# Kernel optimization log

Measured on AMD Instinct MI355X. Metric: run time of the kernel, lower is better.

Reference implementation:

```python
import jax, jax.numpy as jnp
import numpy as np

N_NODES = 8192
IN_F = 256
OUT_F = 256
ALPHA = 0.2  # LeakyReLU negative slope


def setup_inputs() -> dict:
    key = jax.random.key(0)
    k1, k2, k3, k4 = jax.random.split(key, 4)
    X = jax.random.normal(k1, (N_NODES, IN_F), dtype=jnp.float32)
    A = jax.random.randint(k2, (N_NODES, N_NODES), 0, 2, dtype=jnp.int32)
    # torch nn.Linear weight layout: (out_features, in_features)
    W = jax.random.normal(k3, (OUT_F, IN_F), dtype=jnp.float32) * (1.0 / np.sqrt(IN_F))
    r = jax.random.normal(k4, (2 * OUT_F, 1), dtype=jnp.float32)
    return {"X": X, "A": A, "W": W, "r": r}


def reference(X, A, W, r):
    # Wh = X @ W^T  -> (N, F_out)
    Wh = X @ W.T
    # Split r so that cat([Wh_i, Wh_j]) @ r == Wh_i @ r_src + Wh_j @ r_dst
    F_out = Wh.shape[-1]
    r_src = r[:F_out, 0]   # (F,)
    r_dst = r[F_out:, 0]   # (F,)
    s_i = Wh @ r_src       # (N,)
    s_j = Wh @ r_dst       # (N,)
    e = s_i[:, None] + s_j[None, :]                      # (N, N)
    e = jnp.where(e >= 0, e, ALPHA * e)                  # LeakyReLU
    e = jnp.where(A == 0, -jnp.inf, e)                   # mask non-edges
    attention = jax.nn.softmax(e, axis=1)                # row-wise softmax
    output = attention @ Wh                              # (N, F_out)
    return jax.nn.gelu(output, approximate=False)        # torch F.gelu (exact)
```

## Files before the change

kernel.cpp:

```cpp
#include <hip/hip_runtime.h>
#include <hip/hip_bf16.h>

#define N_NODES 8192
#define NF      256
#define L2E     1.44269504088896341f

typedef __attribute__((ext_vector_type(8))) short short8;
typedef __attribute__((ext_vector_type(4))) short short4v;
typedef __attribute__((ext_vector_type(4))) float floatx4;

static __device__ __forceinline__ float bf2f(short s) {
    return __uint_as_float(((unsigned)(unsigned short)s) << 16);
}
static __device__ __forceinline__ short f2bf_rn(float f) {
    unsigned u = __float_as_uint(f) + 0x8000u;
    return (short)(u >> 16);
}
struct bfpair { short hi, lo; };
static __device__ __forceinline__ bfpair split_bf(float x) {
    bfpair p;
    p.hi = f2bf_rn(x);
    p.lo = f2bf_rn(x - bf2f(p.hi));
    return p;
}
static __device__ __forceinline__ void async16(const void* g, void* l) {
    __builtin_amdgcn_global_load_lds(
        (const __attribute__((address_space(1))) unsigned*)g,
        (__attribute__((address_space(3))) unsigned*)l, 16, 0, 0);
}

__global__ __launch_bounds__(256) void kx_split(const float* __restrict__ W,
                                                short* __restrict__ Whi,
                                                short* __restrict__ Wlo) {
    #pragma unroll
    for (int e = 0; e < 4; ++e) {
        const int i = blockIdx.x * 1024 + e * 256 + threadIdx.x;
        bfpair p = split_bf(W[i]);
        Whi[i] = p.hi;
        Wlo[i] = p.lo;
    }
}

__global__ __launch_bounds__(512) void k1_gemm(const float* __restrict__ X,
                                               const short* __restrict__ Whi,
                                               const short* __restrict__ Wlo,
                                               const float* __restrict__ r,
                                               short* __restrict__ WhT,
                                               float* __restrict__ sp_src,
                                               float* __restrict__ sp_dst) {
    __shared__ float Xs[32 * 256];

    const int tid = threadIdx.x;
    const int w = tid >> 6, lane = tid & 63;
    const int q = lane >> 4, m = lane & 15;
    const int rh = w >> 2, cq = w & 3;
    const int i_base = blockIdx.x * 32;

    #pragma unroll
    for (int v = 0; v < 4; ++v) {
        const int rowv = w * 4 + v;
        const int c = lane ^ (rowv & 7);
        async16(X + (size_t)(i_base + rowv) * NF + c * 4, &Xs[rowv * 256]);
    }
    __syncthreads();

    floatx4 acc[4] = {};
    const int xrow = rh * 16 + m;
    const int r7 = xrow & 7;
    #pragma unroll
    for (int ks = 0; ks < 8; ++ks) {
        const int c0 = ks * 8 + q * 2;
        float4 f0 = *(const float4*)(&Xs[xrow * 256 + ((c0 ^ r7) * 4)]);
        float4 f1 = *(const float4*)(&Xs[xrow * 256 + (((c0 + 1) ^ r7) * 4)]);
        const float xsv[8] = {f0.x, f0.y, f0.z, f0.w, f1.x, f1.y, f1.z, f1.w};
        short8 xh, xl;
        #pragma unroll
        for (int c = 0; c < 8; ++c) {
            bfpair p = split_bf(xsv[c]);
            xh[c] = p.hi; xl[c] = p.lo;
        }
        #pragma unroll
        for (int nt = 0; nt < 4; ++nt) {
            const int n = cq * 64 + nt * 16 + m;
            short8 wh = *(const short8*)(Whi + n * NF + ks * 32 + q * 8);
            short8 wl = *(const short8*)(Wlo + n * NF + ks * 32 + q * 8);
            acc[nt] = __builtin_amdgcn_mfma_f32_16x16x32_bf16(xh, wh, acc[nt], 0, 0, 0);
            acc[nt] = __builtin_amdgcn_mfma_f32_16x16x32_bf16(xl, wh, acc[nt], 0, 0, 0);
            acc[nt] = __builtin_amdgcn_mfma_f32_16x16x32_bf16(xh, wl, acc[nt], 0, 0, 0);
        }
    }

    const int i0 = i_base + rh * 16 + q * 4;
    float vs[4] = {0.f, 0.f, 0.f, 0.f}, vd[4] = {0.f, 0.f, 0.f, 0.f};
    #pragma unroll
    for (int nt = 0; nt < 4; ++nt) {
        const int n = cq * 64 + nt * 16 + m;
        short4v v;
        #pragma unroll
        for (int r2 = 0; r2 < 4; ++r2) v[r2] = f2bf_rn(acc[nt][r2]);
        *(short4v*)(WhT + (size_t)n * N_NODES + i0) = v;
        const float rs = r[n], rd = r[NF + n];
        #pragma unroll
        for (int r2 = 0; r2 < 4; ++r2) {
            vs[r2] = fmaf(acc[nt][r2], rs, vs[r2]);
            vd[r2] = fmaf(acc[nt][r2], rd, vd[r2]);
        }
    }
    #pragma unroll
    for (int mask = 1; mask <= 8; mask <<= 1) {
        #pragma unroll
        for (int r2 = 0; r2 < 4; ++r2) {
            vs[r2] += __shfl_xor(vs[r2], mask);
            vd[r2] += __shfl_xor(vd[r2], mask);
        }
    }
    if (m == 0) {
        #pragma unroll
        for (int r2 = 0; r2 < 4; ++r2) {
            sp_src[cq * N_NODES + i0 + r2] = vs[r2];
            sp_dst[cq * N_NODES + i0 + r2] = vd[r2];
        }
    }
}

__global__ __launch_bounds__(256) void k2_sv(const float* __restrict__ sp_src,
                                             const float* __restrict__ sp_dst,
                                             float* __restrict__ s_src,
                                             float* __restrict__ s_dst,
                                             float* __restrict__ pmax) {
    __shared__ float red[256];
    const int tid = threadIdx.x;
    const int i = blockIdx.x * 256 + tid;
    float ss = 0.f, sd = 0.f;
    #pragma unroll
    for (int nb = 0; nb < 4; ++nb) {
        ss += sp_src[nb * N_NODES + i];
        sd += sp_dst[nb * N_NODES + i];
    }
    s_src[i] = ss;
    s_dst[i] = sd;
    red[tid] = sd;
    __syncthreads();
    for (int off = 128; off > 0; off >>= 1) {
        if (tid < off) red[tid] = fmaxf(red[tid], red[tid + off]);
        __syncthreads();
    }
    if (tid == 0) pmax[blockIdx.x] = red[0];
}

__global__ __launch_bounds__(512) void k3_bits(const int* __restrict__ Adj,
                                               unsigned* __restrict__ mask) {
    const int w = threadIdx.x >> 6, lane = threadIdx.x & 63;
    const int row = blockIdx.x * 8 + w;
    const int* Ar = Adj + (size_t)row * N_NODES;
    unsigned long long* Mr = (unsigned long long*)(mask + (size_t)row * 256);
    for (int it = 0; it < 128; ++it) {
        const int v = Ar[it * 64 + lane];
        const unsigned long long b = __ballot(v != 0);
        if (lane == 0) Mr[it] = b;
    }
}

static __device__ __forceinline__ void pgroupb(const unsigned bits, const int sh,
                                               const floatx4 t,
                                               const float s_i, const float d_i,
                                               float* p) {
    #pragma unroll
    for (int c = 0; c < 4; ++c) {
        float sum = s_i + t[c];
        float lr  = fmaxf(sum, 0.2f * sum);
        float pp  = __builtin_amdgcn_exp2f(fmaf(lr, L2E, d_i));
        p[c] = ((bits >> (sh + c)) & 1u) ? pp : 0.0f;
    }
}

__global__ __launch_bounds__(512, 4) void k4_attn(const unsigned* __restrict__ Abits,
                                                  const short* __restrict__ WhT,
                                                  const float* __restrict__ s_dst,
                                                  const float* __restrict__ s_src,
                                                  const float* __restrict__ pmax,
                                                  float* __restrict__ pden,
                                                  float* __restrict__ outacc) {
    __shared__ short Bs[2][256][64];
    __shared__ float ts[2048];

    const int tid = threadIdx.x;
    const int w = tid >> 6, lane = tid & 63;
    const int q = lane >> 4, m = lane & 15;
    const int rh = w >> 1, ch = w & 1;
    const int ib = blockIdx.x & 127;
    const int jh = blockIdx.x >> 7;
    const int i0 = ib * 64;
    const int jbase = jh * 2048;
    const int row = i0 + rh * 16 + m;
    const int q8 = q * 8;

    float M = pmax[0];
    #pragma unroll
    for (int b = 1; b < 32; ++b) M = fmaxf(M, pmax[b]);
    const float s_i = s_src[row];
    const float e0 = s_i + M;
    const float d_i = -fmaxf(e0, 0.2f * e0) * L2E;

    const int srow = lane >> 3;
    const int scc = (lane & 7) ^ srow;
    const short* gB[4];
    #pragma unroll
    for (int v = 0; v < 4; ++v)
        gB[v] = WhT + (size_t)(w * 32 + v * 8 + srow) * N_NODES + jbase + scc * 8;

    const unsigned* Mp = Abits + (size_t)row * 256 + (jbase >> 5);

    floatx4 acc[8];
    #pragma unroll
    for (int nt = 0; nt < 8; ++nt) acc[nt] = (floatx4){0.f, 0.f, 0.f, 0.f};
    float den = 0.f;

    async16(s_dst + jbase + w * 256 + lane * 4, &ts[w * 256]);
    #pragma unroll
    for (int v = 0; v < 4; ++v)
        async16(gB[v], &Bs[0][w * 32 + v * 8][0]);
    uint2 mk = *(const uint2*)(Mp);
    __syncthreads();

    for (int s = 0; s < 32; ++s) {
        const int cur = s & 1;

        short* dstb = &Bs[cur ^ 1][0][0];
        const int gn = ((s + 1) & 31) * 64;
        #pragma unroll
        for (int v = 0; v < 4; ++v)
            async16(gB[v] + gn, dstb + (w * 32 + v * 8) * 64);
        __builtin_amdgcn_sched_barrier(0);

        uint2 nmk = *(const uint2*)(Mp + ((s + 1) & 31) * 2);
        __builtin_amdgcn_sched_barrier(0);

        const int gt = s * 64;
        floatx4 t0 = *(const floatx4*)(ts + gt + q8);
        floatx4 t1 = *(const floatx4*)(ts + gt + q8 + 4);
        floatx4 t2 = *(const floatx4*)(ts + gt + 32 + q8);
        floatx4 t3 = *(const floatx4*)(ts + gt + 32 + q8 + 4);

        float p[16];
        pgroupb(mk.x, q8,     t0, s_i, d_i, p);
        pgroupb(mk.x, q8 + 4, t1, s_i, d_i, p + 4);
        pgroupb(mk.y, q8,     t2, s_i, d_i, p + 8);
        pgroupb(mk.y, q8 + 4, t3, s_i, d_i, p + 12);

        short8 af0, af1;
        #pragma unroll
        for (int c = 0; c < 8; ++c) { af0[c] = f2bf_rn(p[c]); af1[c] = f2bf_rn(p[8 + c]); }
        #pragma unroll
        for (int c = 0; c < 16; ++c) den += p[c];

        const short* Bb = &Bs[cur][0][0];
        __builtin_amdgcn_s_setprio(1);
        #pragma unroll
        for (int nt = 0; nt < 8; ++nt) {
            const int n = ch * 128 + nt * 16 + m;
            const int sw = m & 7;
            short8 b0 = *(const short8*)(Bb + n * 64 + ((q ^ sw) * 8));
            short8 b1 = *(const short8*)(Bb + n * 64 + (((4 + q) ^ sw) * 8));
            acc[nt] = __builtin_amdgcn_mfma_f32_16x16x32_bf16(af0, b0, acc[nt], 0, 0, 0);
            acc[nt] = __builtin_amdgcn_mfma_f32_16x16x32_bf16(af1, b1, acc[nt], 0, 0, 0);
        }
        __builtin_amdgcn_s_setprio(0);

        __builtin_amdgcn_sched_barrier(0);
        asm volatile("s_waitcnt vmcnt(1)" ::: "memory");
        __builtin_amdgcn_s_barrier();

        mk = nmk;
    }

    den += __shfl_xor(den, 16);
    den += __shfl_xor(den, 32);
    if (ch == 0 && q == 0) pden[jh * N_NODES + row] = den;

    #pragma unroll
    for (int nt = 0; nt < 8; ++nt) {
        #pragma unroll
        for (int rg = 0; rg < 4; ++rg) {
            const int orow = i0 + rh * 16 + q * 4 + rg;
            const int n = ch * 128 + nt * 16 + m;
            atomicAdd(&outacc[(size_t)orow * NF + n], acc[nt][rg]);
        }
    }
}

__global__ __launch_bounds__(256) void k5_fin(const float* __restrict__ pden,
                                              float* __restrict__ out) {
    const int gid = blockIdx.x * 256 + threadIdx.x;
    const int row = gid >> 5;
    const int c0 = (gid & 31) * 8;
    const float d = (pden[row] + pden[N_NODES + row]) +
                    (pden[2 * N_NODES + row] + pden[3 * N_NODES + row]);
    const float inv = 1.0f / fmaxf(d, 1e-30f);
    float* p = out + (size_t)row * NF + c0;
    float4 v0 = *(const float4*)(p);
    float4 v1 = *(const float4*)(p + 4);
    float xs[8] = {v0.x, v0.y, v0.z, v0.w, v1.x, v1.y, v1.z, v1.w};
    #pragma unroll
    for (int c = 0; c < 8; ++c) {
        const float x = xs[c] * inv;
        xs[c] = 0.5f * x * (1.0f + erff(x * 0.70710678118f));
    }
    *(float4*)(p)     = (float4){xs[0], xs[1], xs[2], xs[3]};
    *(float4*)(p + 4) = (float4){xs[4], xs[5], xs[6], xs[7]};
}

extern "C" void kernel_launch(void* const* d_in, const int* in_sizes, int n_in,
                              void* d_out, int out_size, void* d_ws, size_t ws_size,
                              hipStream_t stream) {
    const float* X = (const float*)d_in[0];
    const int*   A = (const int*)d_in[1];
    const float* W = (const float*)d_in[2];
    const float* r = (const float*)d_in[3];
    float* out = (float*)d_out;

    char* wsp = (char*)d_ws;
    short* WhT    = (short*)wsp;                    wsp += (size_t)NF * N_NODES * 2;
    short* Whi    = (short*)wsp;                    wsp += NF * NF * 2;
    short* Wlo    = (short*)wsp;                    wsp += NF * NF * 2;
    float* sp_src = (float*)wsp;                    wsp += 4 * N_NODES * 4;
    float* sp_dst = (float*)wsp;                    wsp += 4 * N_NODES * 4;
    float* s_src  = (float*)wsp;                    wsp += N_NODES * 4;
    float* s_dst  = (float*)wsp;                    wsp += N_NODES * 4;
    float* pmax   = (float*)wsp;                    wsp += 256;
    unsigned* Abits = (unsigned*)wsp;
    float* pden   = sp_src;

    hipMemsetAsync(out, 0, (size_t)N_NODES * NF * 4, stream);
    kx_split<<<64, 256, 0, stream>>>(W, Whi, Wlo);
    k1_gemm<<<256, 512, 0, stream>>>(X, Whi, Wlo, r, WhT, sp_src, sp_dst);
    k2_sv<<<32, 256, 0, stream>>>(sp_src, sp_dst, s_src, s_dst, pmax);
    k3_bits<<<1024, 512, 0, stream>>>(A, Abits);
    k4_attn<<<512, 512, 0, stream>>>(Abits, WhT, s_dst, s_src, pmax, pden, out);
    k5_fin<<<1024, 256, 0, stream>>>(pden, out);
}
```

Before: 521.6 us.

## Retile attention kernel to 128-row blocks with 8-way j split; vectorize adjacency bitpacking

The attention kernel now gives each block 128 rows, one 16-row stripe per wave, covering all 256 output columns, and splits the j range into 8 chunks of 1024 instead of 4 of 2048. Each B tile loaded into shared memory is therefore reused across twice as many rows, and each wave holds 16 accumulator tiles. The cost is more accumulator registers, twice as many atomic adds into the output, and 8 partial denominators for the final kernel to sum. Separately, the adjacency bitmask kernel now has each thread pack 32 entries with int4 loads instead of a per-wave ballot loop, to get wider memory accesses. The pden scratch area now holds 8×N floats and relies on sp_src and sp_dst being contiguous, which is fragile.

```diff
diff --git a/kernel.cpp b/kernel.cpp
--- a/kernel.cpp
+++ b/kernel.cpp
@@ -148,17 +148,20 @@
     if (tid == 0) pmax[blockIdx.x] = red[0];
 }
 
-__global__ __launch_bounds__(512) void k3_bits(const int* __restrict__ Adj,
+__global__ __launch_bounds__(256) void k3_bits(const int* __restrict__ Adj,
                                                unsigned* __restrict__ mask) {
-    const int w = threadIdx.x >> 6, lane = threadIdx.x & 63;
-    const int row = blockIdx.x * 8 + w;
-    const int* Ar = Adj + (size_t)row * N_NODES;
-    unsigned long long* Mr = (unsigned long long*)(mask + (size_t)row * 256);
-    for (int it = 0; it < 128; ++it) {
-        const int v = Ar[it * 64 + lane];
-        const unsigned long long b = __ballot(v != 0);
-        if (lane == 0) Mr[it] = b;
-    }
+    const int gid = blockIdx.x * 256 + threadIdx.x;
+    const int4* src = (const int4*)Adj + (size_t)gid * 8;
+    unsigned b = 0;
+    #pragma unroll
+    for (int c = 0; c < 8; ++c) {
+        const int4 v = src[c];
+        b |= (v.x != 0 ? 1u : 0u) << (c * 4);
+        b |= (v.y != 0 ? 1u : 0u) << (c * 4 + 1);
+        b |= (v.z != 0 ? 1u : 0u) << (c * 4 + 2);
+        b |= (v.w != 0 ? 1u : 0u) << (c * 4 + 3);
+    }
+    mask[gid] = b;
 }
 
 static __device__ __forceinline__ void pgroupb(const unsigned bits, const int sh,
@@ -182,16 +185,16 @@
                                                   float* __restrict__ pden,
                                                   float* __restrict__ outacc) {
     __shared__ short Bs[2][256][64];
-    __shared__ float ts[2048];
+    __shared__ float ts[1024];
 
     const int tid = threadIdx.x;
     const int w = tid >> 6, lane = tid & 63;
     const int q = lane >> 4, m = lane & 15;
-    const int rh = w >> 1, ch = w & 1;
-    const int ib = blockIdx.x & 127;
-    const int jh = blockIdx.x >> 7;
-    const int i0 = ib * 64;
-    const int jbase = jh * 2048;
+    const int rh = w;
+    const int ib = blockIdx.x & 63;
+    const int jh = blockIdx.x >> 6;
+    const int i0 = ib * 128;
+    const int jbase = jh * 1024;
     const int row = i0 + rh * 16 + m;
     const int q8 = q * 8;
 
@@ -211,61 +214,71 @@
 
     const unsigned* Mp = Abits + (size_t)row * 256 + (jbase >> 5);
 
-    floatx4 acc[8];
-    #pragma unroll
-    for (int nt = 0; nt < 8; ++nt) acc[nt] = (floatx4){0.f, 0.f, 0.f, 0.f};
+    floatx4 acc[16];
+    #pragma unroll
+    for (int nt = 0; nt < 16; ++nt) acc[nt] = (floatx4){0.f, 0.f, 0.f, 0.f};
     float den = 0.f;
 
-    async16(s_dst + jbase + w * 256 + lane * 4, &ts[w * 256]);
+    if (w < 4) async16(s_dst + jbase + w * 256 + lane * 4, &ts[w * 256]);
     #pragma unroll
     for (int v = 0; v < 4; ++v)
         async16(gB[v], &Bs[0][w * 32 + v * 8][0]);
     uint2 mk = *(const uint2*)(Mp);
     __syncthreads();
 
-    for (int s = 0; s < 32; ++s) {
+    for (int s = 0; s < 16; ++s) {
         const int cur = s & 1;
 
         short* dstb = &Bs[cur ^ 1][0][0];
-        const int gn = ((s + 1) & 31) * 64;
+        const int gn = ((s + 1) & 15) * 64;
         #pragma unroll
         for (int v = 0; v < 4; ++v)
             async16(gB[v] + gn, dstb + (w * 32 + v * 8) * 64);
         __builtin_amdgcn_sched_barrier(0);
 
-        uint2 nmk = *(const uint2*)(Mp + ((s + 1) & 31) * 2);
+        uint2 nmk = *(const uint2*)(Mp + ((s + 1) & 15) * 2);
         __builtin_amdgcn_sched_barrier(0);
 
         const int gt = s * 64;
-        floatx4 t0 = *(const floatx4*)(ts + gt + q8);
-        floatx4 t1 = *(const floatx4*)(ts + gt + q8 + 4);
-        floatx4 t2 = *(const floatx4*)(ts + gt + 32 + q8);
-        floatx4 t3 = *(const floatx4*)(ts + gt + 32 + q8 + 4);
-
-        float p[16];
-        pgroupb(mk.x, q8,     t0, s_i, d_i, p);
-        pgroupb(mk.x, q8 + 4, t1, s_i, d_i, p + 4);
-        pgroupb(mk.y, q8,     t2, s_i, d_i, p + 8);
-        pgroupb(mk.y, q8 + 4, t3, s_i, d_i, p + 12);
-
-        short8 af0, af1;
-        #pragma unroll
-        for (int c = 0; c < 8; ++c) { af0[c] = f2bf_rn(p[c]); af1[c] = f2bf_rn(p[8 + c]); }
-        #pragma unroll
-        for (int c = 0; c < 16; ++c) den += p[c];
-
         const short* Bb = &Bs[cur][0][0];
-        __builtin_amdgcn_s_setprio(1);
-        #pragma unroll
-        for (int nt = 0; nt < 8; ++nt) {
-            const int n = ch * 128 + nt * 16 + m;
-            const int sw = m & 7;
-            short8 b0 = *(const short8*)(Bb + n * 64 + ((q ^ sw) * 8));
-            short8 b1 = *(const short8*)(Bb + n * 64 + (((4 + q) ^ sw) * 8));
-            acc[nt] = __builtin_amdgcn_mfma_f32_16x16x32_bf16(af0, b0, acc[nt], 0, 0, 0);
-            acc[nt] = __builtin_amdgcn_mfma_f32_16x16x32_bf16(af1, b1, acc[nt], 0, 0, 0);
-        }
-        __builtin_amdgcn_s_setprio(0);
+        const int sw = m & 7;
+
+        {
+            floatx4 t0 = *(const floatx4*)(ts + gt + q8);
+            floatx4 t1 = *(const floatx4*)(ts + gt + q8 + 4);
+            float p[8];
+            pgroupb(mk.x, q8,     t0, s_i, d_i, p);
+            pgroupb(mk.x, q8 + 4, t1, s_i, d_i, p + 4);
+            short8 af0;
+            #pragma unroll
+            for (int c = 0; c < 8; ++c) { af0[c] = f2bf_rn(p[c]); den += p[c]; }
+            __builtin_amdgcn_s_setprio(1);
+            #pragma unroll
+            for (int nt = 0; nt < 16; ++nt) {
+                const int n = nt * 16 + m;
+                short8 b0 = *(const short8*)(Bb + n * 64 + ((q ^ sw) * 8));
+                acc[nt] = __builtin_amdgcn_mfma_f32_16x16x32_bf16(af0, b0, acc[nt], 0, 0, 0);
+            }
+            __builtin_amdgcn_s_setprio(0);
+        }
+        {
+            floatx4 t2 = *(const floatx4*)(ts + gt + 32 + q8);
+            floatx4 t3 = *(const floatx4*)(ts + gt + 32 + q8 + 4);
+            float p[8];
+            pgroupb(mk.y, q8,     t2, s_i, d_i, p);
+            pgroupb(mk.y, q8 + 4, t3, s_i, d_i, p + 4);
+            short8 af1;
+            #pragma unroll
+            for (int c = 0; c < 8; ++c) { af1[c] = f2bf_rn(p[c]); den += p[c]; }
+            __builtin_amdgcn_s_setprio(1);
+            #pragma unroll
+            for (int nt = 0; nt < 16; ++nt) {
+                const int n = nt * 16 + m;
+                short8 b1 = *(const short8*)(Bb + n * 64 + (((4 + q) ^ sw) * 8));
+                acc[nt] = __builtin_amdgcn_mfma_f32_16x16x32_bf16(af1, b1, acc[nt], 0, 0, 0);
+            }
+            __builtin_amdgcn_s_setprio(0);
+        }
 
         __builtin_amdgcn_sched_barrier(0);
         asm volatile("s_waitcnt vmcnt(1)" ::: "memory");
@@ -276,14 +289,14 @@
 
     den += __shfl_xor(den, 16);
     den += __shfl_xor(den, 32);
-    if (ch == 0 && q == 0) pden[jh * N_NODES + row] = den;
-
-    #pragma unroll
-    for (int nt = 0; nt < 8; ++nt) {
+    if (q == 0) pden[jh * N_NODES + row] = den;
+
+    #pragma unroll
+    for (int nt = 0; nt < 16; ++nt) {
         #pragma unroll
         for (int rg = 0; rg < 4; ++rg) {
             const int orow = i0 + rh * 16 + q * 4 + rg;
-            const int n = ch * 128 + nt * 16 + m;
+            const int n = nt * 16 + m;
             atomicAdd(&outacc[(size_t)orow * NF + n], acc[nt][rg]);
         }
     }
@@ -294,8 +307,10 @@
     const int gid = blockIdx.x * 256 + threadIdx.x;
     const int row = gid >> 5;
     const int c0 = (gid & 31) * 8;
-    const float d = (pden[row] + pden[N_NODES + row]) +
-                    (pden[2 * N_NODES + row] + pden[3 * N_NODES + row]);
+    const float d = ((pden[row] + pden[N_NODES + row]) +
+                     (pden[2 * N_NODES + row] + pden[3 * N_NODES + row])) +
+                    ((pden[4 * N_NODES + row] + pden[5 * N_NODES + row]) +
+                     (pden[6 * N_NODES + row] + pden[7 * N_NODES + row]));
     const float inv = 1.0f / fmaxf(d, 1e-30f);
     float* p = out + (size_t)row * NF + c0;
     float4 v0 = *(const float4*)(p);
@@ -335,7 +350,7 @@
     kx_split<<<64, 256, 0, stream>>>(W, Whi, Wlo);
     k1_gemm<<<256, 512, 0, stream>>>(X, Whi, Wlo, r, WhT, sp_src, sp_dst);
     k2_sv<<<32, 256, 0, stream>>>(sp_src, sp_dst, s_src, s_dst, pmax);
-    k3_bits<<<1024, 512, 0, stream>>>(A, Abits);
+    k3_bits<<<8192, 256, 0, stream>>>(A, Abits);
     k4_attn<<<512, 512, 0, stream>>>(Abits, WhT, s_dst, s_src, pmax, pden, out);
     k5_fin<<<1024, 256, 0, stream>>>(pden, out);
 }
```

Result: faster. 482.8 us (-7.4%).
